# Performance work log

Measured on AMD Instinct MI355X. Metric: run time of the kernel, lower is better.

Reference implementation:

```python
import jax, jax.numpy as jnp
import numpy as np

B, T, C, H = 8, 2048, 1024, 128  # batch, seq (== block_size), embed dim, head size


def setup_inputs() -> dict:
    key = jax.random.key(0)
    kx, kq, kk, kv = jax.random.split(key, 4)
    x = jax.random.normal(kx, (B, T, C), dtype=jnp.float32)
    # torch Linear(no bias) weights: [head_size, in_features], applied as x @ W.T
    s = 1.0 / np.sqrt(C)
    Wq = jax.random.normal(kq, (H, C), dtype=jnp.float32) * s
    Wk = jax.random.normal(kk, (H, C), dtype=jnp.float32) * s
    Wv = jax.random.normal(kv, (H, C), dtype=jnp.float32) * s
    return {"x": x, "Wq": Wq, "Wk": Wk, "Wv": Wv}


def reference(x, Wq, Wk, Wv):
    # projections: [B,T,C] @ [C,H] -> [B,T,H]
    q = jnp.einsum('btc,hc->bth', x, Wq)
    k = jnp.einsum('btc,hc->bth', x, Wk)
    v = jnp.einsum('btc,hc->bth', x, Wv)
    scale = k.shape[-1] ** -0.5
    # scores [B,T,T], causal mask, softmax in fp32 (autocast disabled in original)
    scores = jnp.einsum('bqh,bkh->bqk', q, k) * scale
    causal = jnp.tril(jnp.ones((T, T), dtype=bool))
    scores = jnp.where(causal, scores, -jnp.inf)
    attn = jax.nn.softmax(scores.astype(jnp.float32), axis=-1)
    # dropout_rate = 0.0 -> identity
    out = jnp.einsum('bqk,bkh->bqh', attn.astype(v.dtype), v)
    return out
```

## Files before the change

kernel.cpp:

```cpp
#include <hip/hip_runtime.h>
#include <hip/hip_bf16.h>

constexpr int NB = 8;
constexpr int T  = 2048;
constexpr int C  = 1024;
constexpr int Hd = 128;

typedef short bf16x8 __attribute__((ext_vector_type(8)));
typedef float floatx4 __attribute__((ext_vector_type(4)));

__device__ __forceinline__ ushort f2bf(float x) {
    return __builtin_bit_cast(ushort, __float2bfloat16(x));
}
__device__ __forceinline__ float bf2f(ushort u) {
    unsigned int x = ((unsigned int)u) << 16;
    return __builtin_bit_cast(float, x);
}
__device__ __forceinline__ unsigned pk2(float a, float b) {
    return ((unsigned)f2bf(a)) | (((unsigned)f2bf(b)) << 16);
}
__device__ __forceinline__ void async16(ushort* lds, const ushort* g) {
    __builtin_amdgcn_global_load_lds(
        (const __attribute__((address_space(1))) unsigned int*)g,
        (__attribute__((address_space(3))) unsigned int*)lds, 16, 0, 0);
}

__global__ __launch_bounds__(256) void convert_xw(
    const float* __restrict__ X, const float* __restrict__ Wq,
    const float* __restrict__ Wk, const float* __restrict__ Wv,
    ushort* __restrict__ Xb, ushort* __restrict__ Wb)
{
    int bid = blockIdx.x;
    if (bid < 8192) {
        size_t i = ((size_t)bid * 256 + threadIdx.x) * 8;
        float4 a = *(const float4*)&X[i];
        float4 b = *(const float4*)&X[i + 4];
        bf16x8 o;
        o[0] = (short)f2bf(a.x); o[1] = (short)f2bf(a.y);
        o[2] = (short)f2bf(a.z); o[3] = (short)f2bf(a.w);
        o[4] = (short)f2bf(b.x); o[5] = (short)f2bf(b.y);
        o[6] = (short)f2bf(b.z); o[7] = (short)f2bf(b.w);
        *(bf16x8*)&Xb[i] = o;
    } else {
        int g = (bid - 8192) * 256 + threadIdx.x;
        size_t base = (size_t)g * 8;
        int sel = (int)(base >> 17);
        const float* W = sel == 0 ? Wq : (sel == 1 ? Wk : Wv);
        float s = (sel == 0) ? 0.12751744f : 1.0f;
        size_t off = base - (size_t)sel * 131072;
        float4 a = *(const float4*)&W[off];
        float4 b = *(const float4*)&W[off + 4];
        bf16x8 o;
        o[0] = (short)f2bf(a.x * s); o[1] = (short)f2bf(a.y * s);
        o[2] = (short)f2bf(a.z * s); o[3] = (short)f2bf(a.w * s);
        o[4] = (short)f2bf(b.x * s); o[5] = (short)f2bf(b.y * s);
        o[6] = (short)f2bf(b.z * s); o[7] = (short)f2bf(b.w * s);
        *(bf16x8*)&Wb[base] = o;
    }
}

__global__ __launch_bounds__(256) void qkv_gemm(
    const ushort* __restrict__ Xb, const ushort* __restrict__ Wb,
    ushort* __restrict__ Qo, ushort* __restrict__ Ko, ushort* __restrict__ Vt)
{
    __shared__ ushort SM[12288];
    ushort* Al = SM;
    ushort* Bl = SM + 8192;
    const int m0 = blockIdx.x * 128;
    const int n0 = blockIdx.y * 64;
    const int tid = threadIdx.x, lane = tid & 63, wave = tid >> 6;
    const int quad = lane >> 4, colL = lane & 15;
    const int wm = (wave & 1) * 64, wn = (wave >> 1) * 32;
    const int lr = lane >> 3;
    const int lcs = ((lane & 7) ^ (lr & 7)) * 8;

    floatx4 accT[2][4] = {};

    for (int k0 = 0; k0 < C; k0 += 64) {
        for (int t = 0; t < 4; ++t) {
            int q = wave * 4 + t;
            async16(&Al[q * 512 + lane * 8],
                    &Xb[(size_t)(m0 + q * 8 + lr) * C + k0 + lcs]);
        }
        for (int t = 0; t < 2; ++t) {
            int q = wave * 2 + t;
            async16(&Bl[q * 512 + lane * 8],
                    &Wb[(size_t)(n0 + q * 8 + lr) * C + k0 + lcs]);
        }
        __syncthreads();

        bf16x8 af[2][4], bfr[2][2];
        for (int kk = 0; kk < 2; ++kk) {
            for (int mt = 0; mt < 4; ++mt)
                af[kk][mt] = *(const bf16x8*)
                    &Al[(wm + mt * 16 + colL) * 64 + (((kk * 4 + quad) ^ (colL & 7))) * 8];
            for (int nt = 0; nt < 2; ++nt)
                bfr[kk][nt] = *(const bf16x8*)
                    &Bl[(wn + nt * 16 + colL) * 64 + (((kk * 4 + quad) ^ (colL & 7))) * 8];
        }
        for (int kk = 0; kk < 2; ++kk)
            for (int nt = 0; nt < 2; ++nt)
                for (int mt = 0; mt < 4; ++mt)
                    accT[nt][mt] = __builtin_amdgcn_mfma_f32_16x16x32_bf16(
                        bfr[kk][nt], af[kk][mt], accT[nt][mt], 0, 0, 0);
        __syncthreads();
    }

    const int sel = n0 >> 7;
    const int h0 = n0 & 127;
    if (sel < 2) {
        ushort* dst = sel == 0 ? Qo : Ko;
        for (int nt = 0; nt < 2; ++nt)
            for (int mt = 0; mt < 4; ++mt) {
                int row = m0 + wm + mt * 16 + colL;
                int h = h0 + wn + nt * 16 + quad * 4;
                uint2 pk;
                pk.x = pk2(accT[nt][mt][0], accT[nt][mt][1]);
                pk.y = pk2(accT[nt][mt][2], accT[nt][mt][3]);
                *(uint2*)&dst[(size_t)row * Hd + h] = pk;
            }
    } else {
        ushort* TL = SM;
        for (int nt = 0; nt < 2; ++nt)
            for (int mt = 0; mt < 4; ++mt) {
                int t = wm + mt * 16 + colL;
                int h = wn + nt * 16 + quad * 4;
                uint2 pk;
                pk.x = pk2(accT[nt][mt][0], accT[nt][mt][1]);
                pk.y = pk2(accT[nt][mt][2], accT[nt][mt][3]);
                *(uint2*)&TL[t * 68 + h] = pk;
            }
        __syncthreads();
        const int b = m0 >> 11, tb = m0 & 2047;
        const int h = tid & 63, tq = tid >> 6;
        for (int st = 0; st < 4; ++st) {
            int t0 = tq * 32 + st * 8;
            bf16x8 o;
            for (int jx = 0; jx < 8; ++jx)
                o[jx] = (short)TL[(t0 + jx) * 68 + h];
            *(bf16x8*)&Vt[((size_t)b * Hd + h0 + h) * T + tb + t0] = o;
        }
    }
}

__global__ __launch_bounds__(256, 2) void attn_partial(
    const ushort* __restrict__ Q, const ushort* __restrict__ Kg,
    const ushort* __restrict__ Vt, ushort* __restrict__ Opart,
    float* __restrict__ mpart, float* __restrict__ lpart)
{
    __shared__ ushort Kl[128 * 128];
    __shared__ ushort Vl[128 * 128];
    __shared__ ushort Pl[4][2048];

    const int tid = threadIdx.x, lane = tid & 63, wave = tid >> 6;
    const int quad = lane >> 4, colL = lane & 15;

    int id = blockIdx.x;
    int b = id / 136;
    int rem = id - b * 136;
    int j = 15;
    while (rem >= j + 1) { rem -= (j + 1); --j; }
    int c = rem;
    const int q0 = j * 128;
    const int k0 = c * 128;
    const bool diag = (c == j);

    {
        int r = tid >> 4, p = tid & 15;
        for (int t = 0; t < 8; ++t) {
            int row = t * 16 + r;
            async16(&Kl[t * 2048 + tid * 8],
                    &Kg[((size_t)b * T + k0 + row) * Hd + ((p ^ (row & 15)) * 8)]);
        }
        for (int t = 0; t < 8; ++t) {
            int hrow = t * 16 + r;
            async16(&Vl[t * 2048 + tid * 8],
                    &Vt[((size_t)b * Hd + hrow) * T + k0 + ((p ^ (hrow & 15)) * 8)]);
        }
    }

    bf16x8 qa[2][4];
    for (int qg = 0; qg < 2; ++qg) {
        const ushort* qp =
            &Q[((size_t)b * T + q0 + wave * 32 + qg * 16 + colL) * Hd + quad * 8];
        for (int ks = 0; ks < 4; ++ks)
            qa[qg][ks] = *(const bf16x8*)&qp[ks * 32];
    }

    __syncthreads();

    floatx4 accST[2][8] = {};
    for (int ks = 0; ks < 4; ++ks)
        for (int kt = 0; kt < 8; ++kt) {
            bf16x8 kb = *(const bf16x8*)
                &Kl[(kt * 16 + colL) * 128 + (((ks * 4 + quad) ^ colL) * 8)];
            accST[0][kt] = __builtin_amdgcn_mfma_f32_16x16x32_bf16(
                kb, qa[0][ks], accST[0][kt], 0, 0, 0);
            accST[1][kt] = __builtin_amdgcn_mfma_f32_16x16x32_bf16(
                kb, qa[1][ks], accST[1][kt], 0, 0, 0);
        }

    if (diag) {
        for (int qg = 0; qg < 2; ++qg) {
            int qglob = q0 + wave * 32 + qg * 16 + colL;
            for (int kt = 0; kt < 8; ++kt)
                for (int rr = 0; rr < 4; ++rr) {
                    int keyg = k0 + kt * 16 + quad * 4 + rr;
                    if (keyg > qglob) accST[qg][kt][rr] = -__builtin_inff();
                }
        }
    }

    float m_r[2], l_r[2];
    for (int qg = 0; qg < 2; ++qg) {
        float mx = accST[qg][0][0];
        for (int kt = 0; kt < 8; ++kt)
            for (int rr = 0; rr < 4; ++rr)
                mx = fmaxf(mx, accST[qg][kt][rr]);
        mx = fmaxf(mx, __shfl_xor(mx, 16, 64));
        mx = fmaxf(mx, __shfl_xor(mx, 32, 64));
        m_r[qg] = mx;
        l_r[qg] = 0.f;
    }

    ushort* Plw = Pl[wave];
    floatx4 OaccT[2][8] = {};
    for (int kh = 0; kh < 2; ++kh) {
        for (int qg = 0; qg < 2; ++qg) {
            int q = qg * 16 + colL;
            for (int ktl = 0; ktl < 4; ++ktl) {
                floatx4 sv = accST[qg][kh * 4 + ktl];
                float p0 = __builtin_amdgcn_exp2f(sv[0] - m_r[qg]);
                float p1 = __builtin_amdgcn_exp2f(sv[1] - m_r[qg]);
                float p2 = __builtin_amdgcn_exp2f(sv[2] - m_r[qg]);
                float p3 = __builtin_amdgcn_exp2f(sv[3] - m_r[qg]);
                l_r[qg] += (p0 + p1) + (p2 + p3);
                int chunk = ktl * 2 + (quad >> 1);
                uint2 pk;
                pk.x = pk2(p0, p1);
                pk.y = pk2(p2, p3);
                *(uint2*)&Plw[q * 64 + ((chunk ^ (q & 7)) * 8) + (quad & 1) * 4] = pk;
            }
        }
        for (int ksl = 0; ksl < 2; ++ksl) {
            int ks = kh * 2 + ksl;
            bf16x8 pf[2];
            for (int qg = 0; qg < 2; ++qg) {
                int q = qg * 16 + colL;
                pf[qg] = *(const bf16x8*)
                    &Plw[q * 64 + (((ksl * 4 + quad) ^ (q & 7)) * 8)];
            }
            for (int mh = 0; mh < 8; ++mh) {
                bf16x8 vb = *(const bf16x8*)
                    &Vl[(mh * 16 + colL) * 128 + (((ks * 4 + quad) ^ colL) * 8)];
                OaccT[0][mh] = __builtin_amdgcn_mfma_f32_16x16x32_bf16(
                    vb, pf[0], OaccT[0][mh], 0, 0, 0);
                OaccT[1][mh] = __builtin_amdgcn_mfma_f32_16x16x32_bf16(
                    vb, pf[1], OaccT[1][mh], 0, 0, 0);
            }
        }
    }

    for (int qg = 0; qg < 2; ++qg) {
        float s = l_r[qg];
        s += __shfl_xor(s, 16, 64);
        s += __shfl_xor(s, 32, 64);
        l_r[qg] = s;
    }

    const int slot = b * 136 + (j * (j + 1)) / 2 + c;
    ushort* Op = &Opart[(size_t)slot * 16384];
    for (int qg = 0; qg < 2; ++qg) {
        int q = wave * 32 + qg * 16 + colL;
        for (int mh = 0; mh < 8; ++mh) {
            uint2 pk;
            pk.x = pk2(OaccT[qg][mh][0], OaccT[qg][mh][1]);
            pk.y = pk2(OaccT[qg][mh][2], OaccT[qg][mh][3]);
            *(uint2*)&Op[q * 128 + mh * 16 + quad * 4] = pk;
        }
        if (quad == 0) {
            mpart[(size_t)slot * 128 + q] = m_r[qg];
            lpart[(size_t)slot * 128 + q] = l_r[qg];
        }
    }
}

__global__ __launch_bounds__(256) void attn_combine(
    const ushort* __restrict__ Opart, const float* __restrict__ mpart,
    const float* __restrict__ lpart, float* __restrict__ out)
{
    const int j = 15 - blockIdx.x, b = blockIdx.y;
    const int nch = j + 1;
    const int sbase = b * 136 + (j * (j + 1)) / 2;
    const int t = threadIdx.x;
    const int row = blockIdx.z * 32 + (t >> 3);
    const int h0 = (t & 7) * 16;

    float M = -__builtin_inff();
    for (int c = 0; c < nch; ++c)
        M = fmaxf(M, mpart[(size_t)(sbase + c) * 128 + row]);
    float ltot = 0.f;
    for (int c = 0; c < nch; ++c)
        ltot += lpart[(size_t)(sbase + c) * 128 + row] *
                __builtin_amdgcn_exp2f(mpart[(size_t)(sbase + c) * 128 + row] - M);

    float o[16];
    for (int i = 0; i < 16; ++i) o[i] = 0.f;
    for (int c = 0; c < nch; ++c) {
        float wgt = __builtin_amdgcn_exp2f(mpart[(size_t)(sbase + c) * 128 + row] - M);
        const ushort* Op = &Opart[(size_t)(sbase + c) * 16384 + row * 128 + h0];
        for (int x = 0; x < 2; ++x) {
            bf16x8 v = *(const bf16x8*)&Op[x * 8];
            for (int i2 = 0; i2 < 8; ++i2)
                o[x * 8 + i2] += bf2f((ushort)v[i2]) * wgt;
        }
    }
    float inv = 1.0f / ltot;
    float* dst = &out[((size_t)(b * T) + j * 128 + row) * Hd + h0];
    for (int i = 0; i < 16; ++i) dst[i] = o[i] * inv;
}

extern "C" void kernel_launch(void* const* d_in, const int* in_sizes, int n_in,
                              void* d_out, int out_size, void* d_ws, size_t ws_size,
                              hipStream_t stream) {
    const float* x  = (const float*)d_in[0];
    const float* Wq = (const float*)d_in[1];
    const float* Wk = (const float*)d_in[2];
    const float* Wv = (const float*)d_in[3];
    float* out = (float*)d_out;

    char* w = (char*)d_ws;
    ushort* Xb = (ushort*)w;
    ushort* Wb = (ushort*)(w + (size_t)33554432);
    ushort* Opart = (ushort*)w;
    float* mpart = (float*)(w + (size_t)35651584);
    float* lpart = (float*)(w + (size_t)35651584 + 557056);
    w += (size_t)35651584 + 2 * 557056;
    ushort* Qb  = (ushort*)w;  w += (size_t)NB * T * Hd * 2;
    ushort* Kb  = (ushort*)w;  w += (size_t)NB * T * Hd * 2;
    ushort* Vtb = (ushort*)w;  w += (size_t)NB * T * Hd * 2;

    convert_xw<<<8384, 256, 0, stream>>>(x, Wq, Wk, Wv, Xb, Wb);
    qkv_gemm<<<dim3(128, 6), 256, 0, stream>>>(Xb, Wb, Qb, Kb, Vtb);
    attn_partial<<<1088, 256, 0, stream>>>(Qb, Kb, Vtb, Opart, mpart, lpart);
    attn_combine<<<dim3(16, 8, 4), 256, 0, stream>>>(Opart, mpart, lpart, out);
}
```

Before: 166.9 us.

## Share one LDS buffer for K and V in attention; remap QKV GEMM blocks

The attention partial kernel now reuses a single shared-memory buffer for K and then V. V is loaded only after the score MFMAs finish, and its load overlaps the first exp/P-store phase. The smaller LDS footprint is meant to let three blocks run per CU (launch bounds raised to 3). Separately, the QKV GEMM uses a 1D grid with a swizzled block index so that blocks sharing X rows across the 8 XCDs are grouped for better cache reuse. The cost is extra barriers and V-load latency that now sits on the critical path after QK^T.

Result: no change. 169.0 us (+1.3%).

```diff
diff --git a/kernel.cpp b/kernel.cpp
--- a/kernel.cpp
+++ b/kernel.cpp
@@ -66,8 +66,10 @@
     __shared__ ushort SM[12288];
     ushort* Al = SM;
     ushort* Bl = SM + 8192;
-    const int m0 = blockIdx.x * 128;
-    const int n0 = blockIdx.y * 64;
+    const int id = blockIdx.x;
+    const int xg = id & 7, s = id >> 3;
+    const int m0 = ((s & 15) * 8 + xg) * 128;
+    const int n0 = (s >> 4) * 64;
     const int tid = threadIdx.x, lane = tid & 63, wave = tid >> 6;
     const int quad = lane >> 4, colL = lane & 15;
     const int wm = (wave & 1) * 64, wn = (wave >> 1) * 32;
@@ -143,13 +145,12 @@
     }
 }
 
-__global__ __launch_bounds__(256, 2) void attn_partial(
+__global__ __launch_bounds__(256, 3) void attn_partial(
     const ushort* __restrict__ Q, const ushort* __restrict__ Kg,
     const ushort* __restrict__ Vt, ushort* __restrict__ Opart,
     float* __restrict__ mpart, float* __restrict__ lpart)
 {
-    __shared__ ushort Kl[128 * 128];
-    __shared__ ushort Vl[128 * 128];
+    __shared__ ushort KVl[128 * 128];
     __shared__ ushort Pl[4][2048];
 
     const int tid = threadIdx.x, lane = tid & 63, wave = tid >> 6;
@@ -169,13 +170,8 @@
         int r = tid >> 4, p = tid & 15;
         for (int t = 0; t < 8; ++t) {
             int row = t * 16 + r;
-            async16(&Kl[t * 2048 + tid * 8],
+            async16(&KVl[t * 2048 + tid * 8],
                     &Kg[((size_t)b * T + k0 + row) * Hd + ((p ^ (row & 15)) * 8)]);
-        }
-        for (int t = 0; t < 8; ++t) {
-            int hrow = t * 16 + r;
-            async16(&Vl[t * 2048 + tid * 8],
-                    &Vt[((size_t)b * Hd + hrow) * T + k0 + ((p ^ (hrow & 15)) * 8)]);
         }
     }
 
@@ -193,7 +189,7 @@
     for (int ks = 0; ks < 4; ++ks)
         for (int kt = 0; kt < 8; ++kt) {
             bf16x8 kb = *(const bf16x8*)
-                &Kl[(kt * 16 + colL) * 128 + (((ks * 4 + quad) ^ colL) * 8)];
+                &KVl[(kt * 16 + colL) * 128 + (((ks * 4 + quad) ^ colL) * 8)];
             accST[0][kt] = __builtin_amdgcn_mfma_f32_16x16x32_bf16(
                 kb, qa[0][ks], accST[0][kt], 0, 0, 0);
             accST[1][kt] = __builtin_amdgcn_mfma_f32_16x16x32_bf16(
@@ -223,41 +219,85 @@
         l_r[qg] = 0.f;
     }
 
+    __syncthreads();
+
+    {
+        int r = tid >> 4, p = tid & 15;
+        for (int t = 0; t < 8; ++t) {
+            int hrow = t * 16 + r;
+            async16(&KVl[t * 2048 + tid * 8],
+                    &Vt[((size_t)b * Hd + hrow) * T + k0 + ((p ^ (hrow & 15)) * 8)]);
+        }
+    }
+
     ushort* Plw = Pl[wave];
+    for (int qg = 0; qg < 2; ++qg) {
+        int q = qg * 16 + colL;
+        for (int ktl = 0; ktl < 4; ++ktl) {
+            floatx4 sv = accST[qg][ktl];
+            float p0 = __builtin_amdgcn_exp2f(sv[0] - m_r[qg]);
+            float p1 = __builtin_amdgcn_exp2f(sv[1] - m_r[qg]);
+            float p2 = __builtin_amdgcn_exp2f(sv[2] - m_r[qg]);
+            float p3 = __builtin_amdgcn_exp2f(sv[3] - m_r[qg]);
+            l_r[qg] += (p0 + p1) + (p2 + p3);
+            int chunk = ktl * 2 + (quad >> 1);
+            uint2 pk;
+            pk.x = pk2(p0, p1);
+            pk.y = pk2(p2, p3);
+            *(uint2*)&Plw[q * 64 + ((chunk ^ (q & 7)) * 8) + (quad & 1) * 4] = pk;
+        }
+    }
+
+    __syncthreads();
+
     floatx4 OaccT[2][8] = {};
-    for (int kh = 0; kh < 2; ++kh) {
+    for (int ksl = 0; ksl < 2; ++ksl) {
+        bf16x8 pf[2];
         for (int qg = 0; qg < 2; ++qg) {
             int q = qg * 16 + colL;
-            for (int ktl = 0; ktl < 4; ++ktl) {
-                floatx4 sv = accST[qg][kh * 4 + ktl];
-                float p0 = __builtin_amdgcn_exp2f(sv[0] - m_r[qg]);
-                float p1 = __builtin_amdgcn_exp2f(sv[1] - m_r[qg]);
-                float p2 = __builtin_amdgcn_exp2f(sv[2] - m_r[qg]);
-                float p3 = __builtin_amdgcn_exp2f(sv[3] - m_r[qg]);
-                l_r[qg] += (p0 + p1) + (p2 + p3);
-                int chunk = ktl * 2 + (quad >> 1);
-                uint2 pk;
-                pk.x = pk2(p0, p1);
-                pk.y = pk2(p2, p3);
-                *(uint2*)&Plw[q * 64 + ((chunk ^ (q & 7)) * 8) + (quad & 1) * 4] = pk;
-            }
-        }
-        for (int ksl = 0; ksl < 2; ++ksl) {
-            int ks = kh * 2 + ksl;
-            bf16x8 pf[2];
-            for (int qg = 0; qg < 2; ++qg) {
-                int q = qg * 16 + colL;
-                pf[qg] = *(const bf16x8*)
-                    &Plw[q * 64 + (((ksl * 4 + quad) ^ (q & 7)) * 8)];
-            }
-            for (int mh = 0; mh < 8; ++mh) {
-                bf16x8 vb = *(const bf16x8*)
-                    &Vl[(mh * 16 + colL) * 128 + (((ks * 4 + quad) ^ colL) * 8)];
-                OaccT[0][mh] = __builtin_amdgcn_mfma_f32_16x16x32_bf16(
-                    vb, pf[0], OaccT[0][mh], 0, 0, 0);
-                OaccT[1][mh] = __builtin_amdgcn_mfma_f32_16x16x32_bf16(
-                    vb, pf[1], OaccT[1][mh], 0, 0, 0);
-            }
+            pf[qg] = *(const bf16x8*)
+                &Plw[q * 64 + (((ksl * 4 + quad) ^ (q & 7)) * 8)];
+        }
+        for (int mh = 0; mh < 8; ++mh) {
+            bf16x8 vb = *(const bf16x8*)
+                &KVl[(mh * 16 + colL) * 128 + (((ksl * 4 + quad) ^ colL) * 8)];
+            OaccT[0][mh] = __builtin_amdgcn_mfma_f32_16x16x32_bf16(
+                vb, pf[0], OaccT[0][mh], 0, 0, 0);
+            OaccT[1][mh] = __builtin_amdgcn_mfma_f32_16x16x32_bf16(
+                vb, pf[1], OaccT[1][mh], 0, 0, 0);
+        }
+    }
+    for (int qg = 0; qg < 2; ++qg) {
+        int q = qg * 16 + colL;
+        for (int ktl = 0; ktl < 4; ++ktl) {
+            floatx4 sv = accST[qg][4 + ktl];
+            float p0 = __builtin_amdgcn_exp2f(sv[0] - m_r[qg]);
+            float p1 = __builtin_amdgcn_exp2f(sv[1] - m_r[qg]);
+            float p2 = __builtin_amdgcn_exp2f(sv[2] - m_r[qg]);
+            float p3 = __builtin_amdgcn_exp2f(sv[3] - m_r[qg]);
+            l_r[qg] += (p0 + p1) + (p2 + p3);
+            int chunk = ktl * 2 + (quad >> 1);
+            uint2 pk;
+            pk.x = pk2(p0, p1);
+            pk.y = pk2(p2, p3);
+            *(uint2*)&Plw[q * 64 + ((chunk ^ (q & 7)) * 8) + (quad & 1) * 4] = pk;
+        }
+    }
+    for (int ksl = 0; ksl < 2; ++ksl) {
+        int ks = 2 + ksl;
+        bf16x8 pf[2];
+        for (int qg = 0; qg < 2; ++qg) {
+            int q = qg * 16 + colL;
+            pf[qg] = *(const bf16x8*)
+                &Plw[q * 64 + (((ksl * 4 + quad) ^ (q & 7)) * 8)];
+        }
+        for (int mh = 0; mh < 8; ++mh) {
+            bf16x8 vb = *(const bf16x8*)
+                &KVl[(mh * 16 + colL) * 128 + (((ks * 4 + quad) ^ colL) * 8)];
+            OaccT[0][mh] = __builtin_amdgcn_mfma_f32_16x16x32_bf16(
+                vb, pf[0], OaccT[0][mh], 0, 0, 0);
+            OaccT[1][mh] = __builtin_amdgcn_mfma_f32_16x16x32_bf16(
+                vb, pf[1], OaccT[1][mh], 0, 0, 0);
         }
     }
 
@@ -341,7 +381,7 @@
     ushort* Vtb = (ushort*)w;  w += (size_t)NB * T * Hd * 2;
 
     convert_xw<<<8384, 256, 0, stream>>>(x, Wq, Wk, Wv, Xb, Wb);
-    qkv_gemm<<<dim3(128, 6), 256, 0, stream>>>(Xb, Wb, Qb, Kb, Vtb);
+    qkv_gemm<<<768, 256, 0, stream>>>(Xb, Wb, Qb, Kb, Vtb);
     attn_partial<<<1088, 256, 0, stream>>>(Qb, Kb, Vtb, Opart, mpart, lpart);
     attn_combine<<<dim3(16, 8, 4), 256, 0, stream>>>(Opart, mpart, lpart, out);
 }
```
